# Optimization experiments

Measured on AMD Instinct MI355X. Metric: run time of the kernel, lower is better.

Reference implementation:

```python
import jax, jax.numpy as jnp
import numpy as np

DIM = 1024
HEADS = 16
EPS = 1e-5  # torch nn.LayerNorm default


def layernorm(x, g, b):
    # normalize over last axis
    mu = jnp.mean(x, axis=-1, keepdims=True)
    var = jnp.mean(jnp.square(x - mu), axis=-1, keepdims=True)
    return (x - mu) * jax.lax.rsqrt(var + EPS) * g + b


def setup_inputs() -> dict:
    key = jax.random.key(0)
    ks = jax.random.split(key, 8)
    B, N, C = 4, 1024, DIM
    s = 1.0 / np.sqrt(C)
    return {
        "x": jax.random.normal(ks[0], (B, N, C), jnp.float32),
        "qkv_w": jax.random.normal(ks[1], (3 * C, C), jnp.float32) * s,
        "qkv_b": jnp.zeros((3 * C,), jnp.float32),
        "q_norm_g": jnp.ones((C,), jnp.float32),
        "q_norm_b": jnp.zeros((C,), jnp.float32),
        "k_norm_g": jnp.ones((C,), jnp.float32),
        "k_norm_b": jnp.zeros((C,), jnp.float32),
        "proj_w": jax.random.normal(ks[2], (C, C), jnp.float32) * s,
        "proj_b": jnp.zeros((C,), jnp.float32),
    }


def reference(x, qkv_w, qkv_b, q_norm_g, q_norm_b, k_norm_g, k_norm_b, proj_w, proj_b):
    B, N, C = x.shape
    H = HEADS
    D = C // H
    scale = D ** -0.5

    qkv = x @ qkv_w.T + qkv_b                      # [B,N,3C]
    qkv = qkv.reshape(B, N, 3, H, D)
    q, k, v = qkv[:, :, 0], qkv[:, :, 1], qkv[:, :, 2]  # [B,N,H,D]

    # qk_normalization: LayerNorm over flattened (H*D)=C per token
    q = layernorm(q.reshape(B, N, C), q_norm_g, q_norm_b).reshape(B, N, H, D)
    k = layernorm(k.reshape(B, N, C), k_norm_g, k_norm_b).reshape(B, N, H, D)

    # attention: [B,H,N,N]
    attn = jnp.einsum('bqhd,bkhd->bhqk', q * scale, k)
    attn = jax.nn.softmax(attn, axis=-1)
    out = jnp.einsum('bhqk,bkhd->bqhd', attn, v).reshape(B, N, C)
    return out @ proj_w.T + proj_b
```

## Files before the change

kernel.cpp:

```cpp
#include <hip/hip_runtime.h>
#include <hip/hip_bf16.h>

#define C_DIM 1024
#define HEADS 16

typedef __bf16 bf16x8 __attribute__((ext_vector_type(8)));
typedef float f32x4 __attribute__((ext_vector_type(4)));

static __device__ __forceinline__ unsigned short f2bf(float f) {
  unsigned int u = __builtin_bit_cast(unsigned int, f);
  u += 0x7FFFu + ((u >> 16) & 1u);
  return (unsigned short)(u >> 16);
}

static __device__ __forceinline__ float bf2f(unsigned short u) {
  unsigned int v = ((unsigned int)u) << 16;
  return __builtin_bit_cast(float, v);
}

static __device__ __forceinline__ void glds16(const unsigned short* g,
                                              unsigned short* l) {
  __builtin_amdgcn_global_load_lds(
      (const __attribute__((address_space(1))) unsigned int*)g,
      (__attribute__((address_space(3))) unsigned int*)l, 16, 0, 0);
}

__global__ void cast_bf16_kernel(const float* __restrict__ src,
                                 unsigned short* __restrict__ dst, int n4) {
  int i = blockIdx.x * blockDim.x + threadIdx.x;
  if (i >= n4) return;
  float4 v = *reinterpret_cast<const float4*>(src + (size_t)i * 4);
  ushort4 o;
  o.x = f2bf(v.x); o.y = f2bf(v.y); o.z = f2bf(v.z); o.w = f2bf(v.w);
  *reinterpret_cast<ushort4*>(dst + (size_t)i * 4) = o;
}

template <bool BF16_OUT>
__global__ __launch_bounds__(256, 2) void gemm_nt(
    const unsigned short* __restrict__ A, const unsigned short* __restrict__ B,
    const float* __restrict__ bias, void* __restrict__ Cout,
    int M, int N, int K) {
  __shared__ __align__(16) unsigned short As[128 * 64];
  __shared__ __align__(16) unsigned short Bs[128 * 64];
  const int tid = threadIdx.x;
  const int lane = tid & 63;
  const int wave = tid >> 6;
  const int wm = wave >> 1, wn = wave & 1;
  const int g = lane >> 4, r = lane & 15;
  const int bm = blockIdx.x * 128, bn = blockIdx.y * 128;

  f32x4 acc[4][4] = {};

  for (int k0 = 0; k0 < K; k0 += 64) {
    __syncthreads();
#pragma unroll
    for (int i = 0; i < 4; ++i) {
      int cb = i * 256 + wave * 64;
      int c = cb + lane;
      int row = c >> 3, col = (c & 7) * 8;
      glds16(&A[(size_t)(bm + row) * K + k0 + col], &As[cb * 8]);
      glds16(&B[(size_t)(bn + row) * K + k0 + col], &Bs[cb * 8]);
    }
    __syncthreads();

    bf16x8 af[4][2], bf[4][2];
#pragma unroll
    for (int m = 0; m < 4; ++m) {
      af[m][0] = *reinterpret_cast<const bf16x8*>(&As[(wm * 64 + m * 16 + r) * 64 + g * 8]);
      af[m][1] = *reinterpret_cast<const bf16x8*>(&As[(wm * 64 + m * 16 + r) * 64 + 32 + g * 8]);
    }
#pragma unroll
    for (int n = 0; n < 4; ++n) {
      bf[n][0] = *reinterpret_cast<const bf16x8*>(&Bs[(wn * 64 + n * 16 + r) * 64 + g * 8]);
      bf[n][1] = *reinterpret_cast<const bf16x8*>(&Bs[(wn * 64 + n * 16 + r) * 64 + 32 + g * 8]);
    }
#pragma unroll
    for (int m = 0; m < 4; ++m)
#pragma unroll
      for (int n = 0; n < 4; ++n) {
        acc[m][n] = __builtin_amdgcn_mfma_f32_16x16x32_bf16(af[m][0], bf[n][0], acc[m][n], 0, 0, 0);
        acc[m][n] = __builtin_amdgcn_mfma_f32_16x16x32_bf16(af[m][1], bf[n][1], acc[m][n], 0, 0, 0);
      }
  }

#pragma unroll
  for (int m = 0; m < 4; ++m) {
    int row0 = bm + wm * 64 + m * 16 + g * 4;
#pragma unroll
    for (int n = 0; n < 4; ++n) {
      int col = bn + wn * 64 + n * 16 + r;
      float bv = bias[col];
#pragma unroll
      for (int rr = 0; rr < 4; ++rr) {
        float v = acc[m][n][rr] + bv;
        if (BF16_OUT)
          reinterpret_cast<unsigned short*>(Cout)[(size_t)(row0 + rr) * N + col] = f2bf(v);
        else
          reinterpret_cast<float*>(Cout)[(size_t)(row0 + rr) * N + col] = v;
      }
    }
  }
}

__global__ __launch_bounds__(256) void ln_pack_kernel(
    const unsigned short* __restrict__ qkv, const float* __restrict__ qg,
    const float* __restrict__ qb, const float* __restrict__ kg,
    const float* __restrict__ kb, unsigned short* __restrict__ Q,
    unsigned short* __restrict__ Ko, unsigned short* __restrict__ V) {
  const int t = blockIdx.x;
  const int b = t >> 10, n = t & 1023;
  const int tid = threadIdx.x;
  const int lane = tid & 63, wave = tid >> 6;
  const unsigned short* row = qkv + (size_t)t * 3072;
  ushort4 qu = *reinterpret_cast<const ushort4*>(row + tid * 4);
  ushort4 ku = *reinterpret_cast<const ushort4*>(row + 1024 + tid * 4);
  ushort4 vu = *reinterpret_cast<const ushort4*>(row + 2048 + tid * 4);
  float q0 = bf2f(qu.x), q1 = bf2f(qu.y), q2 = bf2f(qu.z), q3 = bf2f(qu.w);
  float k0 = bf2f(ku.x), k1 = bf2f(ku.y), k2 = bf2f(ku.z), k3 = bf2f(ku.w);

  float qs = q0 + q1 + q2 + q3;
  float qss = q0 * q0 + q1 * q1 + q2 * q2 + q3 * q3;
  float ks = k0 + k1 + k2 + k3;
  float kss = k0 * k0 + k1 * k1 + k2 * k2 + k3 * k3;
#pragma unroll
  for (int m = 1; m < 64; m <<= 1) {
    qs += __shfl_xor(qs, m);
    qss += __shfl_xor(qss, m);
    ks += __shfl_xor(ks, m);
    kss += __shfl_xor(kss, m);
  }
  __shared__ float red[4][4];
  if (lane == 0) {
    red[wave][0] = qs; red[wave][1] = qss; red[wave][2] = ks; red[wave][3] = kss;
  }
  __syncthreads();
  qs = red[0][0] + red[1][0] + red[2][0] + red[3][0];
  qss = red[0][1] + red[1][1] + red[2][1] + red[3][1];
  ks = red[0][2] + red[1][2] + red[2][2] + red[3][2];
  kss = red[0][3] + red[1][3] + red[2][3] + red[3][3];
  const float inv = 1.0f / 1024.0f;
  float qmu = qs * inv, kmu = ks * inv;
  float qrs = rsqrtf(qss * inv - qmu * qmu + 1e-5f);
  float krs = rsqrtf(kss * inv - kmu * kmu + 1e-5f);

  int c0 = tid * 4;
  float4 qg4 = *reinterpret_cast<const float4*>(qg + c0);
  float4 qb4 = *reinterpret_cast<const float4*>(qb + c0);
  float4 kg4 = *reinterpret_cast<const float4*>(kg + c0);
  float4 kb4 = *reinterpret_cast<const float4*>(kb + c0);
  int h = c0 >> 6, d = c0 & 63;
  size_t off = (((size_t)(b * HEADS + h)) * 1024 + n) * 64 + d;
  ushort4 qo, ko, vo;
  qo.x = f2bf(((q0 - qmu) * qrs * qg4.x + qb4.x) * 0.125f);
  qo.y = f2bf(((q1 - qmu) * qrs * qg4.y + qb4.y) * 0.125f);
  qo.z = f2bf(((q2 - qmu) * qrs * qg4.z + qb4.z) * 0.125f);
  qo.w = f2bf(((q3 - qmu) * qrs * qg4.w + qb4.w) * 0.125f);
  ko.x = f2bf((k0 - kmu) * krs * kg4.x + kb4.x);
  ko.y = f2bf((k1 - kmu) * krs * kg4.y + kb4.y);
  ko.z = f2bf((k2 - kmu) * krs * kg4.z + kb4.z);
  ko.w = f2bf((k3 - kmu) * krs * kg4.w + kb4.w);
  vo.x = vu.x; vo.y = vu.y; vo.z = vu.z; vo.w = vu.w;
  *reinterpret_cast<ushort4*>(Q + off) = qo;
  *reinterpret_cast<ushort4*>(Ko + off) = ko;
  *reinterpret_cast<ushort4*>(V + off) = vo;
}

__global__ __launch_bounds__(256) void transpose_v(
    const unsigned short* __restrict__ V, unsigned short* __restrict__ VT) {
  const int bid = blockIdx.x;
  const int bh = bid >> 4, nt = bid & 15;
  const unsigned short* src = V + (size_t)bh * 65536 + nt * 64 * 64;
  unsigned short* dst = VT + (size_t)bh * 65536 + nt * 64;
  __shared__ __align__(16) unsigned short tile[64][68];
  const int tid = threadIdx.x;
#pragma unroll
  for (int i = 0; i < 4; ++i) {
    int idx = i * 256 + tid;
    int row = idx >> 4, c4 = (idx & 15) * 4;
    *reinterpret_cast<ushort4*>(&tile[row][c4]) =
        *reinterpret_cast<const ushort4*>(&src[row * 64 + c4]);
  }
  __syncthreads();
#pragma unroll
  for (int i = 0; i < 4; ++i) {
    int idx = i * 256 + tid;
    int d = idx >> 4, p = (idx & 15) * 4;
    int key0 = 16 * (2 * (p >> 5) + ((p >> 2) & 1)) + 4 * ((p >> 3) & 3);
    ushort4 o;
    o.x = tile[key0][d]; o.y = tile[key0 + 1][d];
    o.z = tile[key0 + 2][d]; o.w = tile[key0 + 3][d];
    *reinterpret_cast<ushort4*>(&dst[(size_t)d * 1024 + p]) = o;
  }
}

__global__ __launch_bounds__(256, 4) void attn_kernel(
    const unsigned short* __restrict__ Q, const unsigned short* __restrict__ K,
    const unsigned short* __restrict__ VT, unsigned short* __restrict__ O) {
  const int blk = blockIdx.x;
  const int bh = blk & 63;
  const int qb = blk >> 6;
  const int tid = threadIdx.x;
  const int lane = tid & 63, wave = tid >> 6;
  const int g = lane >> 4, r = lane & 15;
  const unsigned short* Qh = Q + (size_t)bh * 65536;
  const unsigned short* Kh = K + (size_t)bh * 65536;
  const unsigned short* Vth = VT + (size_t)bh * 65536;
  const int q0 = qb * 64 + wave * 16;

  __shared__ __align__(16) unsigned short KL[2][4096];
  __shared__ __align__(16) unsigned short VL[2][4096];

  bf16x8 bq0 = *reinterpret_cast<const bf16x8*>(&Qh[(q0 + r) * 64 + g * 8]);
  bf16x8 bq1 = *reinterpret_cast<const bf16x8*>(&Qh[(q0 + r) * 64 + 32 + g * 8]);

  f32x4 ao[4] = {};
  float mreg = -1e30f, lreg = 0.f;

  auto STAGE = [&](int b, int kt) {
#pragma unroll
    for (int t = 0; t < 2; ++t) {
      int cb = (wave * 2 + t) * 64;
      int i = cb + lane;
      int row = i >> 3, pcol = i & 7;
      int lc = pcol ^ (row & 7);
      glds16(Kh + (size_t)(kt + row) * 64 + lc * 8, &KL[b][cb * 8]);
      glds16(Vth + (size_t)row * 1024 + kt + lc * 8, &VL[b][cb * 8]);
    }
  };

  STAGE(0, 0);
  __syncthreads();
  int cur = 0;

  for (int kt = 0; kt < 1024; kt += 64) {
    if (kt + 64 < 1024) STAGE(cur ^ 1, kt + 64);
    const unsigned short* KB = KL[cur];
    const unsigned short* VB = VL[cur];
    const int sw = r & 7;

    f32x4 s[4];
#pragma unroll
    for (int j = 0; j < 4; ++j) {
      const int row = 16 * j + r;
      bf16x8 k0 = *reinterpret_cast<const bf16x8*>(&KB[row * 64 + (g ^ sw) * 8]);
      bf16x8 k1 = *reinterpret_cast<const bf16x8*>(&KB[row * 64 + ((4 + g) ^ sw) * 8]);
      f32x4 t = {};
      t = __builtin_amdgcn_mfma_f32_16x16x32_bf16(k0, bq0, t, 0, 0, 0);
      t = __builtin_amdgcn_mfma_f32_16x16x32_bf16(k1, bq1, t, 0, 0, 0);
      s[j] = t;
    }
    float v01 = fmaxf(fmaxf(s[0][0], s[0][1]), fmaxf(s[0][2], s[0][3]));
    float v23 = fmaxf(fmaxf(s[1][0], s[1][1]), fmaxf(s[1][2], s[1][3]));
    float v45 = fmaxf(fmaxf(s[2][0], s[2][1]), fmaxf(s[2][2], s[2][3]));
    float v67 = fmaxf(fmaxf(s[3][0], s[3][1]), fmaxf(s[3][2], s[3][3]));
    float v = fmaxf(fmaxf(v01, v23), fmaxf(v45, v67));
    v = fmaxf(v, __shfl_xor(v, 16));
    v = fmaxf(v, __shfl_xor(v, 32));
    float mnew = fmaxf(mreg, v);
    float fac = __expf(mreg - mnew);
    mreg = mnew;
#pragma unroll
    for (int j = 0; j < 4; ++j)
#pragma unroll
      for (int rr = 0; rr < 4; ++rr) s[j][rr] = __expf(s[j][rr] - mnew);
    float ps = ((s[0][0] + s[0][1]) + (s[0][2] + s[0][3])) +
               ((s[1][0] + s[1][1]) + (s[1][2] + s[1][3])) +
               ((s[2][0] + s[2][1]) + (s[2][2] + s[2][3])) +
               ((s[3][0] + s[3][1]) + (s[3][2] + s[3][3]));
    ps += __shfl_xor(ps, 16);
    ps += __shfl_xor(ps, 32);
    lreg = lreg * fac + ps;
    float facr[4];
#pragma unroll
    for (int rr = 0; rr < 4; ++rr)
      facr[rr] = __shfl(fac, (lane & 48) | (4 * g + rr));
#pragma unroll
    for (int n = 0; n < 4; ++n)
#pragma unroll
      for (int rr = 0; rr < 4; ++rr) ao[n][rr] *= facr[rr];
    uint4 u0, u1;
    asm("v_cvt_pk_bf16_f32 %0, %1, %2" : "=v"(u0.x) : "v"(s[0][0]), "v"(s[0][1]));
    asm("v_cvt_pk_bf16_f32 %0, %1, %2" : "=v"(u0.y) : "v"(s[0][2]), "v"(s[0][3]));
    asm("v_cvt_pk_bf16_f32 %0, %1, %2" : "=v"(u0.z) : "v"(s[1][0]), "v"(s[1][1]));
    asm("v_cvt_pk_bf16_f32 %0, %1, %2" : "=v"(u0.w) : "v"(s[1][2]), "v"(s[1][3]));
    asm("v_cvt_pk_bf16_f32 %0, %1, %2" : "=v"(u1.x) : "v"(s[2][0]), "v"(s[2][1]));
    asm("v_cvt_pk_bf16_f32 %0, %1, %2" : "=v"(u1.y) : "v"(s[2][2]), "v"(s[2][3]));
    asm("v_cvt_pk_bf16_f32 %0, %1, %2" : "=v"(u1.z) : "v"(s[3][0]), "v"(s[3][1]));
    asm("v_cvt_pk_bf16_f32 %0, %1, %2" : "=v"(u1.w) : "v"(s[3][2]), "v"(s[3][3]));
    bf16x8 ap0 = __builtin_bit_cast(bf16x8, u0);
    bf16x8 ap1 = __builtin_bit_cast(bf16x8, u1);
#pragma unroll
    for (int n = 0; n < 4; ++n) {
      const int row = n * 16 + r;
      bf16x8 v0 = *reinterpret_cast<const bf16x8*>(&VB[row * 64 + (g ^ sw) * 8]);
      bf16x8 v1 = *reinterpret_cast<const bf16x8*>(&VB[row * 64 + ((4 + g) ^ sw) * 8]);
      ao[n] = __builtin_amdgcn_mfma_f32_16x16x32_bf16(ap0, v0, ao[n], 0, 0, 0);
      ao[n] = __builtin_amdgcn_mfma_f32_16x16x32_bf16(ap1, v1, ao[n], 0, 0, 0);
    }
    __syncthreads();
    cur ^= 1;
  }

  const int b = bh >> 4, h = bh & 15;
  float lr[4];
#pragma unroll
  for (int rr = 0; rr < 4; ++rr)
    lr[rr] = 1.0f / __shfl(lreg, (lane & 48) | (4 * g + rr));
#pragma unroll
  for (int n = 0; n < 4; ++n)
#pragma unroll
    for (int rr = 0; rr < 4; ++rr) {
      int tok = q0 + 4 * g + rr;
      O[(((size_t)(b * 1024 + tok)) * 16 + h) * 64 + n * 16 + r] =
          f2bf(ao[n][rr] * lr[rr]);
    }
}

__global__ void sentinel_kernel(unsigned short* out, float v) {
  if (threadIdx.x == 0 && blockIdx.x == 0) out[0] = f2bf(v);
}

extern "C" void kernel_launch(void* const* d_in, const int* in_sizes, int n_in,
                              void* d_out, int out_size, void* d_ws, size_t ws_size,
                              hipStream_t stream) {
  const float* x      = (const float*)d_in[0];
  const float* qkv_w  = (const float*)d_in[1];
  const float* qkv_b  = (const float*)d_in[2];
  const float* q_g    = (const float*)d_in[3];
  const float* q_b    = (const float*)d_in[4];
  const float* k_g    = (const float*)d_in[5];
  const float* k_b    = (const float*)d_in[6];
  const float* proj_w = (const float*)d_in[7];
  const float* proj_b = (const float*)d_in[8];

  const int M = in_sizes[0] / C_DIM;
  const int Bb = M / 1024;

  const size_t required = (size_t)M * 3072 * 2 + (size_t)3 * M * 1024 * 2;
  if (ws_size < required) {
    sentinel_kernel<<<1, 64, 0, stream>>>((unsigned short*)d_out, (float)ws_size);
    return;
  }

  unsigned short* qkv_bf = (unsigned short*)d_ws;
  unsigned short* Qb = qkv_bf + (size_t)M * 3072;
  unsigned short* Kb = Qb + (size_t)M * 1024;
  unsigned short* Vb = Kb + (size_t)M * 1024;
  unsigned short* x_bf = Qb;
  unsigned short* qw_bf = Kb;
  unsigned short* AO = qkv_bf;
  unsigned short* VT = qkv_bf + (size_t)M * 1024;
  unsigned short* pw_bf = qkv_bf + (size_t)2 * M * 1024;

  cast_bf16_kernel<<<M * 1024 / 1024, 256, 0, stream>>>(x, x_bf, M * 1024 / 4);
  cast_bf16_kernel<<<3072 * 1024 / 1024, 256, 0, stream>>>(qkv_w, qw_bf, 3072 * 1024 / 4);

  gemm_nt<true><<<dim3(M / 128, 3072 / 128), 256, 0, stream>>>(
      x_bf, qw_bf, qkv_b, qkv_bf, M, 3072, 1024);

  ln_pack_kernel<<<M, 256, 0, stream>>>(qkv_bf, q_g, q_b, k_g, k_b, Qb, Kb, Vb);

  transpose_v<<<Bb * HEADS * 16, 256, 0, stream>>>(Vb, VT);
  cast_bf16_kernel<<<1024 * 1024 / 1024, 256, 0, stream>>>(proj_w, pw_bf, 1024 * 1024 / 4);

  attn_kernel<<<Bb * HEADS * 16, 256, 0, stream>>>(Qb, Kb, VT, AO);

  gemm_nt<false><<<dim3(M / 128, 1024 / 128), 256, 0, stream>>>(
      AO, pw_bf, proj_b, (float*)d_out, M, 1024, 1024);
}
```

Before: 124.5 us.

## Fold log2e into Q scale, lazy softmax rescale, merge cast launches

```diff
diff --git a/kernel.cpp b/kernel.cpp
--- a/kernel.cpp
+++ b/kernel.cpp
@@ -33,6 +33,21 @@
   ushort4 o;
   o.x = f2bf(v.x); o.y = f2bf(v.y); o.z = f2bf(v.z); o.w = f2bf(v.w);
   *reinterpret_cast<ushort4*>(dst + (size_t)i * 4) = o;
+}
+
+__global__ void cast2_kernel(const float* __restrict__ s0,
+                             const float* __restrict__ s1,
+                             unsigned short* __restrict__ d0,
+                             unsigned short* __restrict__ d1, int n40) {
+  int i = blockIdx.x * 256 + threadIdx.x;
+  const float* s;
+  unsigned short* d;
+  if (i < n40) { s = s0; d = d0; }
+  else { s = s1; d = d1; i -= n40; }
+  float4 v = *reinterpret_cast<const float4*>(s + (size_t)i * 4);
+  ushort4 o;
+  o.x = f2bf(v.x); o.y = f2bf(v.y); o.z = f2bf(v.z); o.w = f2bf(v.w);
+  *reinterpret_cast<ushort4*>(d + (size_t)i * 4) = o;
 }
 
 template <bool BF16_OUT>
@@ -151,10 +166,11 @@
   int h = c0 >> 6, d = c0 & 63;
   size_t off = (((size_t)(b * HEADS + h)) * 1024 + n) * 64 + d;
   ushort4 qo, ko, vo;
-  qo.x = f2bf(((q0 - qmu) * qrs * qg4.x + qb4.x) * 0.125f);
-  qo.y = f2bf(((q1 - qmu) * qrs * qg4.y + qb4.y) * 0.125f);
-  qo.z = f2bf(((q2 - qmu) * qrs * qg4.z + qb4.z) * 0.125f);
-  qo.w = f2bf(((q3 - qmu) * qrs * qg4.w + qb4.w) * 0.125f);
+  const float QS = 0.125f * 1.44269504f;
+  qo.x = f2bf(((q0 - qmu) * qrs * qg4.x + qb4.x) * QS);
+  qo.y = f2bf(((q1 - qmu) * qrs * qg4.y + qb4.y) * QS);
+  qo.z = f2bf(((q2 - qmu) * qrs * qg4.z + qb4.z) * QS);
+  qo.w = f2bf(((q3 - qmu) * qrs * qg4.w + qb4.w) * QS);
   ko.x = f2bf((k0 - kmu) * krs * kg4.x + kb4.x);
   ko.y = f2bf((k1 - kmu) * krs * kg4.y + kb4.y);
   ko.z = f2bf((k2 - kmu) * krs * kg4.z + kb4.z);
@@ -249,35 +265,39 @@
       t = __builtin_amdgcn_mfma_f32_16x16x32_bf16(k1, bq1, t, 0, 0, 0);
       s[j] = t;
     }
-    float v01 = fmaxf(fmaxf(s[0][0], s[0][1]), fmaxf(s[0][2], s[0][3]));
-    float v23 = fmaxf(fmaxf(s[1][0], s[1][1]), fmaxf(s[1][2], s[1][3]));
-    float v45 = fmaxf(fmaxf(s[2][0], s[2][1]), fmaxf(s[2][2], s[2][3]));
-    float v67 = fmaxf(fmaxf(s[3][0], s[3][1]), fmaxf(s[3][2], s[3][3]));
-    float v = fmaxf(fmaxf(v01, v23), fmaxf(v45, v67));
+    float a0 = fmaxf(fmaxf(s[0][0], s[0][1]), s[0][2]);
+    float a1 = fmaxf(fmaxf(s[0][3], s[1][0]), s[1][1]);
+    float a2 = fmaxf(fmaxf(s[1][2], s[1][3]), s[2][0]);
+    float a3 = fmaxf(fmaxf(s[2][1], s[2][2]), s[2][3]);
+    float a4 = fmaxf(fmaxf(s[3][0], s[3][1]), s[3][2]);
+    float v = fmaxf(fmaxf(fmaxf(a0, a1), fmaxf(a2, a3)), fmaxf(a4, s[3][3]));
     v = fmaxf(v, __shfl_xor(v, 16));
     v = fmaxf(v, __shfl_xor(v, 32));
-    float mnew = fmaxf(mreg, v);
-    float fac = __expf(mreg - mnew);
-    mreg = mnew;
+    if (!__all((int)(v - mreg <= 8.0f))) {
+      float mnew = fmaxf(mreg, v);
+      float fac = exp2f(mreg - mnew);
+      mreg = mnew;
+      lreg *= fac;
+      float facr[4];
+#pragma unroll
+      for (int rr = 0; rr < 4; ++rr)
+        facr[rr] = __shfl(fac, (lane & 48) | (4 * g + rr));
+#pragma unroll
+      for (int n = 0; n < 4; ++n)
+#pragma unroll
+        for (int rr = 0; rr < 4; ++rr) ao[n][rr] *= facr[rr];
+    }
 #pragma unroll
     for (int j = 0; j < 4; ++j)
 #pragma unroll
-      for (int rr = 0; rr < 4; ++rr) s[j][rr] = __expf(s[j][rr] - mnew);
+      for (int rr = 0; rr < 4; ++rr) s[j][rr] = exp2f(s[j][rr] - mreg);
     float ps = ((s[0][0] + s[0][1]) + (s[0][2] + s[0][3])) +
                ((s[1][0] + s[1][1]) + (s[1][2] + s[1][3])) +
                ((s[2][0] + s[2][1]) + (s[2][2] + s[2][3])) +
                ((s[3][0] + s[3][1]) + (s[3][2] + s[3][3]));
     ps += __shfl_xor(ps, 16);
     ps += __shfl_xor(ps, 32);
-    lreg = lreg * fac + ps;
-    float facr[4];
-#pragma unroll
-    for (int rr = 0; rr < 4; ++rr)
-      facr[rr] = __shfl(fac, (lane & 48) | (4 * g + rr));
-#pragma unroll
-    for (int n = 0; n < 4; ++n)
-#pragma unroll
-      for (int rr = 0; rr < 4; ++rr) ao[n][rr] *= facr[rr];
+    lreg += ps;
     uint4 u0, u1;
     asm("v_cvt_pk_bf16_f32 %0, %1, %2" : "=v"(u0.x) : "v"(s[0][0]), "v"(s[0][1]));
     asm("v_cvt_pk_bf16_f32 %0, %1, %2" : "=v"(u0.y) : "v"(s[0][2]), "v"(s[0][3]));
@@ -352,8 +372,11 @@
   unsigned short* VT = qkv_bf + (size_t)M * 1024;
   unsigned short* pw_bf = qkv_bf + (size_t)2 * M * 1024;
 
-  cast_bf16_kernel<<<M * 1024 / 1024, 256, 0, stream>>>(x, x_bf, M * 1024 / 4);
-  cast_bf16_kernel<<<3072 * 1024 / 1024, 256, 0, stream>>>(qkv_w, qw_bf, 3072 * 1024 / 4);
+  const int n4x = M * 1024 / 4;
+  const int n4w1 = 3072 * 1024 / 4;
+  const int n4w2 = 1024 * 1024 / 4;
+  cast2_kernel<<<(n4x + n4w1) / 256, 256, 0, stream>>>(
+      x, qkv_w, x_bf, qw_bf, n4x);
 
   gemm_nt<true><<<dim3(M / 128, 3072 / 128), 256, 0, stream>>>(
       x_bf, qw_bf, qkv_b, qkv_bf, M, 3072, 1024);
@@ -361,7 +384,8 @@
   ln_pack_kernel<<<M, 256, 0, stream>>>(qkv_bf, q_g, q_b, k_g, k_b, Qb, Kb, Vb);
 
   transpose_v<<<Bb * HEADS * 16, 256, 0, stream>>>(Vb, VT);
-  cast_bf16_kernel<<<1024 * 1024 / 1024, 256, 0, stream>>>(proj_w, pw_bf, 1024 * 1024 / 4);
+
+  cast_bf16_kernel<<<n4w2 / 256, 256, 0, stream>>>(proj_w, pw_bf, n4w2);
 
   attn_kernel<<<Bb * HEADS * 16, 256, 0, stream>>>(Qb, Kb, VT, AO);
 
```

Result: no change. 124.9 us (+0.4%).
